# Kernel tuning notes

Hardware: AMD Instinct MI355X
Metric: run time of the kernel (lower is better)

## Reference

```python
import jax, jax.numpy as jnp
import numpy as np

B, L, V, E, H, DOUT = 32, 128, 30000, 300, 512, 5
NUM_STEPS = 5
WINDOW = 1


def setup_inputs() -> dict:
    key = jax.random.key(0)
    ks = jax.random.split(key, 16)
    def p(k, shape, scale=0.02):
        return jax.random.normal(k, shape, jnp.float32) * scale
    tokens = jax.random.randint(ks[0], (B, L), 1, V)
    lengths = jnp.maximum(jax.random.randint(ks[1], (B,), 1, L + 1), 8)
    embed = p(ks[2], (V, E), 0.1).at[0].set(0.0)  # padding_idx=0 row zeroed
    W0 = p(ks[3], (E, H)); b0 = jnp.zeros((H,), jnp.float32)
    Wg = p(ks[4], (3 * H + E + H, 7 * H)); bg = jnp.zeros((7 * H,), jnp.float32)
    Wgf = p(ks[5], (2 * H, H)); bgf = jnp.zeros((H,), jnp.float32)
    Wfi = p(ks[6], (2 * H, H)); bfi = jnp.zeros((H,), jnp.float32)
    Wgo = p(ks[7], (2 * H, H)); bgo = jnp.zeros((H,), jnp.float32)
    W1 = p(ks[8], (H, 2 * H)); b1 = jnp.zeros((2 * H,), jnp.float32)
    W2 = p(ks[9], (2 * H, DOUT)); b2 = jnp.zeros((DOUT,), jnp.float32)
    return dict(tokens=tokens, lengths=lengths, embed=embed, W0=W0, b0=b0,
                Wg=Wg, bg=bg, Wgf=Wgf, bgf=bgf, Wfi=Wfi, bfi=bfi,
                Wgo=Wgo, bgo=bgo, W1=W1, b1=b1, W2=W2, b2=b2)


def _shift_r(a, k):  # h_{i-k}
    return jnp.pad(a, ((0, 0), (k, 0), (0, 0)))[:, :L]


def _shift_l(a, k):  # h_{i+k}
    return jnp.pad(a, ((0, 0), (0, k), (0, 0)))[:, k:]


def reference(tokens, lengths, embed, W0, b0, Wg, bg, Wgf, bgf, Wfi, bfi,
              Wgo, bgo, W1, b1, W2, b2):
    x = embed[tokens]                                   # [B,L,E]
    mask = (jnp.arange(L)[None, :] < lengths[:, None]).astype(x.dtype)[:, :, None]
    lens = jnp.maximum(lengths.astype(x.dtype), 1.0)[:, None]  # [B,1]
    h = jnp.tanh(x @ W0 + b0) * mask                    # word node init [B,L,H]
    c = jnp.zeros_like(h)
    g = jnp.sum(h, axis=1) / lens                       # global node [B,H]
    cg = jnp.zeros_like(g)

    def step(carry, _):
        h, c, g, cg = carry
        hl = sum(_shift_r(h, k) for k in range(1, WINDOW + 1))
        hr = sum(_shift_l(h, k) for k in range(1, WINDOW + 1))
        gb = jnp.broadcast_to(g[:, None, :], h.shape)
        ctx = jnp.concatenate([hl, h, hr, x, gb], axis=-1)  # [B,L,3H+E+H]
        gates = ctx @ Wg + bg                               # [B,L,7H]
        gi, gl, gf, gr, gs, go, gu = jnp.split(gates, 7, axis=-1)
        nrm = jax.nn.softmax(jnp.stack([gi, gl, gf, gr, gs], 0), axis=0)
        i_, l_, f_, r_, s_ = nrm[0], nrm[1], nrm[2], nrm[3], nrm[4]
        o = jax.nn.sigmoid(go)
        u = jnp.tanh(gu)
        c_new = (l_ * _shift_r(c, 1) + f_ * c + r_ * _shift_l(c, 1)
                 + s_ * cg[:, None, :] + i_ * u) * mask
        h_new = o * jnp.tanh(c_new) * mask
        # global (sentence-state) node update
        h_avg = jnp.sum(h_new, axis=1) / lens
        gcat = jnp.concatenate([g, h_avg], axis=-1)         # [B,2H]
        fg = gcat @ Wgf + bgf                               # [B,H]
        og = jax.nn.sigmoid(gcat @ Wgo + bgo)
        fi = jnp.concatenate([jnp.broadcast_to(g[:, None, :], h_new.shape),
                              h_new], axis=-1) @ Wfi + bfi  # [B,L,H]
        slot_logits = jnp.concatenate([fg[:, None, :], fi], axis=1)  # [B,L+1,H]
        slot_mask = jnp.concatenate([jnp.ones((B, 1, 1), x.dtype), mask], axis=1)
        slot_logits = jnp.where(slot_mask > 0, slot_logits, -1e9)
        w = jax.nn.softmax(slot_logits, axis=1)
        cg_new = w[:, 0] * cg + jnp.sum(w[:, 1:] * c_new, axis=1)
        g_new = og * jnp.tanh(cg_new)
        return (h_new, c_new, g_new, cg_new), None

    (h, c, g, cg), _ = jax.lax.scan(step, (h, c, g, cg), None, length=NUM_STEPS)
    logits = jnp.tanh(g @ W1 + b1) @ W2 + b2            # [B,DOUT]
    return jax.nn.log_softmax(logits, axis=-1)
```

## Files before the change

### kernel.cpp

```cpp
#include <hip/hip_runtime.h>
#include <hip/hip_bf16.h>
#include <math.h>

#define B_ 32
#define L_ 128
#define LP 130
#define E_ 300
#define EP 320
#define H_ 512
#define DOUT_ 5
#define NSTEP 5
#define G7 3584
#define KGATES 1856
#define KFI 512

typedef __hip_bfloat16 bf16;
using bf16x8 = __attribute__((ext_vector_type(8))) __bf16;
using f32x4 = __attribute__((ext_vector_type(4))) float;

__device__ __forceinline__ void gload16(const void* g, void* l) {
  __builtin_amdgcn_global_load_lds(
      (const __attribute__((address_space(1))) void*)g,
      (__attribute__((address_space(3))) void*)l, 16, 0, 0);
}

__global__ void fill_zero(float* __restrict__ p, int n) {
  int i = blockIdx.x * blockDim.x + threadIdx.x;
  if (i < n) p[i] = 0.f;
}

__global__ void mask_lens_kernel(const int* __restrict__ lengths,
                                 float* __restrict__ maskf,
                                 float* __restrict__ invlens) {
  int i = blockIdx.x * blockDim.x + threadIdx.x;
  if (i < B_ * L_) {
    int b = i >> 7, l = i & 127;
    maskf[i] = (l < lengths[b]) ? 1.f : 0.f;
    if (l == 0) invlens[b] = 1.f / fmaxf((float)lengths[b], 1.f);
  }
}

__global__ void embed_bf16_kernel(const int* __restrict__ tokens,
                                  const float* __restrict__ embed,
                                  bf16* __restrict__ xb) {
  int i = blockIdx.x * blockDim.x + threadIdx.x;
  if (i >= B_ * L_ * EP) return;
  int e = i % EP, bl = i / EP;
  float v = (e < E_) ? embed[(size_t)tokens[bl] * E_ + e] : 0.f;
  xb[i] = __float2bfloat16(v);
}

__global__ void fill_pad(bf16* __restrict__ hpad) {
  int i = blockIdx.x * blockDim.x + threadIdx.x;
  if (i >= B_ * 2 * H_) return;
  int hh = i & (H_ - 1);
  int r = (i >> 9) & 1, b = i >> 10;
  hpad[((size_t)(b * LP + r * (LP - 1))) * H_ + hh] = __float2bfloat16(0.f);
}

__global__ __launch_bounds__(256) void transpose_to_bf16(
    const float* __restrict__ W, bf16* __restrict__ Wt, int Kreal, int Ncols,
    int dstStride) {
  __shared__ float tile[64][65];
  const int k0 = blockIdx.x * 64, n0 = blockIdx.y * 64;
  const int t = threadIdx.x;
  const int nn = t & 63, kk0 = t >> 6;
#pragma unroll
  for (int p = 0; p < 16; ++p) {
    int kk = kk0 + p * 4;
    int gk = k0 + kk;
    tile[kk][nn] = (gk < Kreal) ? W[(size_t)gk * Ncols + n0 + nn] : 0.f;
  }
  __syncthreads();
#pragma unroll
  for (int p = 0; p < 2; ++p) {
    int r = (t >> 3) + p * 32;
    int kb = (t & 7) * 8;
    union { ushort h[8]; uint4 v; } u;
#pragma unroll
    for (int e = 0; e < 8; ++e) {
      bf16 b = __float2bfloat16(tile[kb + e][r]);
      u.h[e] = *(ushort*)&b;
    }
    *(uint4*)&Wt[(size_t)(n0 + r) * dstStride + k0 + kb] = u.v;
  }
}

__global__ __launch_bounds__(256) void gemm_mfma_init(
    const bf16* __restrict__ A, const bf16* __restrict__ Bt,
    const float* __restrict__ bias, const float* __restrict__ rowscale,
    bf16* __restrict__ Cout, int N, int KP) {
  __shared__ ushort As[128 * 64];
  __shared__ ushort Bs[128 * 64];
  const int tid = threadIdx.x;
  const int lane = tid & 63;
  const int w = tid >> 6;
  const int wr = w >> 1, wc = w & 1;
  const int nbx = gridDim.x;
  const int nwg = nbx * gridDim.y;
  int id = blockIdx.y * nbx + blockIdx.x;
  if ((nwg & 7) == 0) { int q = nwg >> 3; id = (id & 7) * q + (id >> 3); }
  const int bxi = id % nbx, byi = id / nbx;
  const int rowBase = byi * 128, colBase = bxi * 128;
  const int l15 = lane & 15, l4 = lane >> 4;
  f32x4 acc[4][4] = {};

  const bf16* bP[4];
  const bf16* aP[4];
#pragma unroll
  for (int i = 0; i < 4; ++i) {
    int c = tid + 256 * i;
    int r = c >> 3;
    int ql = (c & 7) ^ (r & 7);
    bP[i] = Bt + (size_t)(colBase + r) * KP + ql * 8;
    aP[i] = A + (size_t)(rowBase + r) * KP + ql * 8;
  }

  const int nIter = KP >> 6;
  for (int t = 0; t < nIter; ++t) {
    int k0 = t * 64;
#pragma unroll
    for (int i = 0; i < 4; ++i) {
      gload16(aP[i] + k0, &As[(tid + 256 * i) * 8]);
      gload16(bP[i] + k0, &Bs[(tid + 256 * i) * 8]);
    }
    __syncthreads();
#pragma unroll
    for (int kh = 0; kh < 2; ++kh) {
      bf16x8 aF[4], bF[4];
#pragma unroll
      for (int m = 0; m < 4; ++m) {
        int row = wr * 64 + m * 16 + l15;
        aF[m] = *(const bf16x8*)&As[row * 64 +
                                    (((kh << 2) + l4) ^ (l15 & 7)) * 8];
      }
#pragma unroll
      for (int n = 0; n < 4; ++n) {
        int row = wc * 64 + n * 16 + l15;
        bF[n] = *(const bf16x8*)&Bs[row * 64 +
                                    (((kh << 2) + l4) ^ (l15 & 7)) * 8];
      }
#pragma unroll
      for (int m = 0; m < 4; ++m)
#pragma unroll
        for (int n = 0; n < 4; ++n)
          acc[m][n] = __builtin_amdgcn_mfma_f32_16x16x32_bf16(
              aF[m], bF[n], acc[m][n], 0, 0, 0);
    }
    __syncthreads();
  }

#pragma unroll
  for (int m = 0; m < 4; ++m) {
#pragma unroll
    for (int n = 0; n < 4; ++n) {
      int col = colBase + wc * 64 + n * 16 + l15;
      float bv = bias[col];
#pragma unroll
      for (int j = 0; j < 4; ++j) {
        int row = rowBase + wr * 64 + m * 16 + l4 * 4 + j;
        float v = tanhf(acc[m][n][j] + bv) * rowscale[row];
        size_t oi = ((size_t)((row >> 7) * LP + (row & 127) + 1)) * H_ + col;
        Cout[oi] = __float2bfloat16(v);
      }
    }
  }
}

__global__ __launch_bounds__(256) void gates_gemm(
    const bf16* __restrict__ hpad, const bf16* __restrict__ xb,
    const bf16* __restrict__ Wgt, const float* __restrict__ bias,
    const float* __restrict__ gg, const int* __restrict__ lengths,
    bf16* __restrict__ gatesb) {
  __shared__ ushort As[64 * 64];
  __shared__ ushort Bs[128 * 64];
  const int tid = threadIdx.x;
  const int lane = tid & 63;
  const int w = tid >> 6;
  int id = blockIdx.y * 28 + blockIdx.x;
  id = (id & 7) * 224 + (id >> 3);
  const int bxi = id % 28, byi = id / 28;
  const int b = byi >> 1, lhalf = byi & 1;
  if (lhalf && lengths[b] <= 64) return;
  const int rowBase = byi * 64;
  const int colBase = bxi * 128;
  const int l15 = lane & 15, l4 = lane >> 4;
  f32x4 acc[4][2] = {};

  const int hRowBase = b * LP + lhalf * 64;
  const int blBase = b * L_ + lhalf * 64;
  const bf16* aP[2];
  const bf16* xP[2];
  const bf16* bP[4];
#pragma unroll
  for (int i = 0; i < 2; ++i) {
    int c = tid + 256 * i;
    int r = c >> 3;
    int ql = (c & 7) ^ (r & 7);
    aP[i] = hpad + (size_t)(hRowBase + r) * H_ + ql * 8;
    xP[i] = xb + (size_t)(blBase + r) * EP + ql * 8;
  }
#pragma unroll
  for (int i = 0; i < 4; ++i) {
    int c = tid + 256 * i;
    int r = c >> 3;
    int ql = (c & 7) ^ (r & 7);
    bP[i] = Wgt + (size_t)(colBase + r) * KGATES + ql * 8;
  }

  auto step_ = [&](const bf16* const* ap, int ko, int kb) {
#pragma unroll
    for (int i = 0; i < 2; ++i)
      gload16(ap[i] + ko, &As[(tid + 256 * i) * 8]);
#pragma unroll
    for (int i = 0; i < 4; ++i)
      gload16(bP[i] + kb, &Bs[(tid + 256 * i) * 8]);
    __syncthreads();
#pragma unroll
    for (int kh = 0; kh < 2; ++kh) {
      bf16x8 aF[4], bF[2];
#pragma unroll
      for (int m = 0; m < 4; ++m) {
        int row = m * 16 + l15;
        aF[m] = *(const bf16x8*)&As[row * 64 +
                                    (((kh << 2) + l4) ^ (l15 & 7)) * 8];
      }
#pragma unroll
      for (int n = 0; n < 2; ++n) {
        int row = w * 32 + n * 16 + l15;
        bF[n] = *(const bf16x8*)&Bs[row * 64 +
                                    (((kh << 2) + l4) ^ (l15 & 7)) * 8];
      }
#pragma unroll
      for (int m = 0; m < 4; ++m)
#pragma unroll
        for (int n = 0; n < 2; ++n)
          acc[m][n] = __builtin_amdgcn_mfma_f32_16x16x32_bf16(
              aF[m], bF[n], acc[m][n], 0, 0, 0);
    }
    __syncthreads();
  };

  for (int t = 0; t < 24; ++t) step_(aP, t * 64, t * 64);
  for (int t = 24; t < 29; ++t) step_(xP, (t - 24) * 64, t * 64);

#pragma unroll
  for (int m = 0; m < 4; ++m) {
#pragma unroll
    for (int n = 0; n < 2; ++n) {
      int col = colBase + w * 32 + n * 16 + l15;
      float bv = bias[col] + gg[(size_t)b * G7 + col];
      bf16 tmp[4];
#pragma unroll
      for (int j = 0; j < 4; ++j)
        tmp[j] = __float2bfloat16(acc[m][n][j] + bv);
      int row0 = rowBase + m * 16 + l4 * 4;
      *(uint2*)&gatesb[((size_t)(row0 >> 2) * G7 + col) * 4] = *(uint2*)tmp;
    }
  }
}

__global__ __launch_bounds__(256) void gvec_gemm(
    const float* __restrict__ g, const float* __restrict__ Wgg,
    const float* __restrict__ Wfi, float* __restrict__ gg,
    float* __restrict__ gfi) {
  __shared__ float vin[H_];
  __shared__ float red[4][64];
  const int b = blockIdx.y;
  for (int i = threadIdx.x; i < H_; i += 256) vin[i] = g[(size_t)b * H_ + i];
  __syncthreads();
  const int o = threadIdx.x & 63, kp = threadIdx.x >> 6;
  const bool isg = blockIdx.x < 56;
  const int n0 = isg ? blockIdx.x * 64 : (blockIdx.x - 56) * 64;
  const float* W = isg ? Wgg : Wfi;
  const int ldw = isg ? G7 : H_;
  float acc = 0.f;
#pragma unroll 4
  for (int k = kp * 128; k < kp * 128 + 128; ++k)
    acc = fmaf(vin[k], W[(size_t)k * ldw + n0 + o], acc);
  red[kp][o] = acc;
  __syncthreads();
  if (threadIdx.x < 64) {
    int t = threadIdx.x;
    float v = red[0][t] + red[1][t] + red[2][t] + red[3][t];
    if (isg) gg[(size_t)b * G7 + n0 + t] = v;
    else gfi[(size_t)b * H_ + n0 + t] = v;
  }
}

__global__ __launch_bounds__(256) void fi_slot_kernel(
    const bf16* __restrict__ hpad, const bf16* __restrict__ Wfit,
    const float* __restrict__ bfi, const float* __restrict__ gfi,
    const float* __restrict__ fg, const float* __restrict__ og,
    const bf16* __restrict__ c_new, const float* __restrict__ cg_old,
    const float* __restrict__ maskf, float* __restrict__ cg_new,
    float* __restrict__ g_new) {
  __shared__ __align__(16) char smem[64 * 129 * 4 + 3072];
  ushort* As = (ushort*)smem;
  ushort* Bs = As + 128 * 64;
  float* sfi = (float*)smem;
  float* part = sfi + 64 * 129;

  const int tid = threadIdx.x;
  const int lane = tid & 63;
  const int w = tid >> 6;
  const int b = blockIdx.y;
  const int colBase = blockIdx.x * 64;
  const int l15 = lane & 15, l4 = lane >> 4;
  f32x4 acc[2][4] = {};

  const bf16* aP[4];
  const bf16* bP[2];
#pragma unroll
  for (int i = 0; i < 4; ++i) {
    int c = tid + 256 * i;
    int r = c >> 3;
    int ql = (c & 7) ^ (r & 7);
    aP[i] = hpad + ((size_t)(b * LP + r + 1)) * H_ + ql * 8;
  }
#pragma unroll
  for (int i = 0; i < 2; ++i) {
    int c = tid + 256 * i;
    int r = c >> 3;
    int ql = (c & 7) ^ (r & 7);
    bP[i] = Wfit + (size_t)(colBase + r) * KFI + ql * 8;
  }

  for (int t = 0; t < 8; ++t) {
    int k0 = t * 64;
#pragma unroll
    for (int i = 0; i < 4; ++i)
      gload16(aP[i] + k0, &As[(tid + 256 * i) * 8]);
#pragma unroll
    for (int i = 0; i < 2; ++i)
      gload16(bP[i] + k0, &Bs[(tid + 256 * i) * 8]);
    __syncthreads();
#pragma unroll
    for (int kh = 0; kh < 2; ++kh) {
      bf16x8 aF[2], bF[4];
#pragma unroll
      for (int m = 0; m < 2; ++m) {
        int row = w * 32 + m * 16 + l15;
        aF[m] = *(const bf16x8*)&As[row * 64 +
                                    (((kh << 2) + l4) ^ (l15 & 7)) * 8];
      }
#pragma unroll
      for (int n = 0; n < 4; ++n) {
        int row = n * 16 + l15;
        bF[n] = *(const bf16x8*)&Bs[row * 64 +
                                    (((kh << 2) + l4) ^ (l15 & 7)) * 8];
      }
#pragma unroll
      for (int m = 0; m < 2; ++m)
#pragma unroll
        for (int n = 0; n < 4; ++n)
          acc[m][n] = __builtin_amdgcn_mfma_f32_16x16x32_bf16(
              aF[m], bF[n], acc[m][n], 0, 0, 0);
    }
    __syncthreads();
  }

#pragma unroll
  for (int m = 0; m < 2; ++m) {
#pragma unroll
    for (int n = 0; n < 4; ++n) {
      int hl_ = n * 16 + l15;
      float bv = bfi[colBase + hl_] + gfi[(size_t)b * H_ + colBase + hl_];
#pragma unroll
      for (int j = 0; j < 4; ++j) {
        int l = w * 32 + m * 16 + l4 * 4 + j;
        sfi[hl_ * 129 + l] = acc[m][n][j] + bv;
      }
    }
  }
  __syncthreads();

  {
    int h = tid & 63, q = tid >> 6;
    int hcol = colBase + h;
    const float* mp = maskf + b * L_;
    float m = -3.0e38f, s = 0.f, tv = 0.f;
    for (int l = q * 32; l < q * 32 + 32; ++l) {
      if (mp[l] > 0.f) {
        float xv = sfi[h * 129 + l];
        float vv = __bfloat162float(c_new[((size_t)(b * L_ + l)) * H_ + hcol]);
        float m2 = fmaxf(m, xv);
        float sc = expf(m - m2);
        float e = expf(xv - m2);
        s = s * sc + e;
        tv = tv * sc + e * vv;
        m = m2;
      }
    }
    part[q * 192 + h] = m;
    part[q * 192 + 64 + h] = s;
    part[q * 192 + 128 + h] = tv;
  }
  __syncthreads();
  if (tid < 64) {
    int hcol = colBase + tid;
    int i0 = b * H_ + hcol;
    float mm = part[tid], s0 = part[64 + tid], t0 = part[128 + tid];
#pragma unroll
    for (int k = 1; k < 4; ++k) {
      float mk = part[k * 192 + tid];
      float m2 = fmaxf(mm, mk);
      float e1 = expf(mm - m2), e2 = expf(mk - m2);
      s0 = s0 * e1 + part[k * 192 + 64 + tid] * e2;
      t0 = t0 * e1 + part[k * 192 + 128 + tid] * e2;
      mm = m2;
    }
    float f = fg[i0];
    float m2 = fmaxf(mm, f);
    float ea = expf(mm - m2), eb = expf(f - m2);
    s0 = s0 * ea + eb;
    t0 = t0 * ea + cg_old[i0] * eb;
    float cgn = t0 / s0;
    float gn = og[i0] * tanhf(cgn);
    cg_new[i0] = cgn;
    g_new[i0] = gn;
  }
}

__global__ __launch_bounds__(512) void cell_mean_kernel(
    const bf16* __restrict__ gates, const bf16* __restrict__ c_old,
    const float* __restrict__ cg_old, const float* __restrict__ maskf,
    const float* __restrict__ invlens, bf16* __restrict__ hpad,
    bf16* __restrict__ c_new, float* __restrict__ havg) {
  __shared__ float part[8][64];
  const int b = blockIdx.y;
  const int h0 = blockIdx.x * 64;
  const int hh = threadIdx.x & 63;
  const int lq = threadIdx.x >> 6;
  const int hcol = h0 + hh;
  const float cgv = cg_old[b * H_ + hcol];
  float s = 0.f;
  for (int it = 0; it < 4; ++it) {
    const int gi = it * 8 + lq;
    const int l0 = gi * 4;
    const size_t gbase = ((size_t)(b * 32 + gi) * G7 + hcol) * 4;
    uint2 gv[7];
#pragma unroll
    for (int gt = 0; gt < 7; ++gt)
      gv[gt] = *(const uint2*)&gates[gbase + (size_t)gt * H_ * 4];
    float crow[6];
#pragma unroll
    for (int jj = 0; jj < 6; ++jj) {
      int l = l0 + jj - 1;
      crow[jj] = (l >= 0 && l < L_)
                     ? __bfloat162float(c_old[((size_t)(b * L_ + l)) * H_ + hcol])
                     : 0.f;
    }
#pragma unroll
    for (int j = 0; j < 4; ++j) {
      int l = l0 + j;
      int bl = b * L_ + l;
      float gl_[7];
#pragma unroll
      for (int gt = 0; gt < 7; ++gt) {
        ushort us = ((const ushort*)&gv[gt])[j];
        bf16 hb;
        *(ushort*)&hb = us;
        gl_[gt] = __bfloat162float(hb);
      }
      float m = fmaxf(fmaxf(fmaxf(gl_[0], gl_[1]), fmaxf(gl_[2], gl_[3])),
                      gl_[4]);
      float ei = expf(gl_[0] - m), el = expf(gl_[1] - m),
            ef = expf(gl_[2] - m), er = expf(gl_[3] - m),
            es = expf(gl_[4] - m);
      float inv = 1.f / (ei + el + ef + er + es);
      float o = 1.f / (1.f + expf(-gl_[5]));
      float u = tanhf(gl_[6]);
      float mk = maskf[bl];
      float cn = (el * crow[j] + ef * crow[j + 1] + er * crow[j + 2] +
                  es * cgv + ei * u) * inv * mk;
      float hn = o * tanhf(cn) * mk;
      c_new[(size_t)bl * H_ + hcol] = __float2bfloat16(cn);
      hpad[((size_t)(b * LP + l + 1)) * H_ + hcol] = __float2bfloat16(hn);
      s += hn;
    }
  }
  part[lq][hh] = s;
  __syncthreads();
  if (threadIdx.x < 64) {
    int t = threadIdx.x;
    float v = 0.f;
#pragma unroll
    for (int k = 0; k < 8; ++k) v += part[k][t];
    havg[b * H_ + h0 + t] = v * invlens[b];
  }
}

__global__ __launch_bounds__(256) void reduce_mean_v2(
    const bf16* __restrict__ hpad, const float* __restrict__ invlens,
    float* __restrict__ outf) {
  __shared__ float sm[4][64];
  int b = blockIdx.y, h0 = blockIdx.x * 64;
  int lg = threadIdx.x >> 6, hh = threadIdx.x & 63;
  float s = 0.f;
  for (int l = lg * 32; l < lg * 32 + 32; ++l)
    s += __bfloat162float(hpad[((size_t)(b * LP + l + 1)) * H_ + h0 + hh]);
  sm[lg][hh] = s;
  __syncthreads();
  if (threadIdx.x < 64) {
    int t = threadIdx.x;
    outf[b * H_ + h0 + t] =
        (sm[0][t] + sm[1][t] + sm[2][t] + sm[3][t]) * invlens[b];
  }
}

__global__ __launch_bounds__(256) void batch_vec_gemm(
    const float* __restrict__ in1, int K1, const float* __restrict__ in2,
    int K2, const float* __restrict__ Wa, const float* __restrict__ ba,
    float* __restrict__ outa, int acta, const float* __restrict__ Wb,
    const float* __restrict__ bb, float* __restrict__ outb, int actb, int N) {
  const float* W = (blockIdx.z == 0) ? Wa : Wb;
  const float* bias = (blockIdx.z == 0) ? ba : bb;
  float* op = (blockIdx.z == 0) ? outa : outb;
  int act = (blockIdx.z == 0) ? acta : actb;
  __shared__ float vin[1024];
  __shared__ float red[4][64];
  const int K = K1 + K2;
  const int n0 = blockIdx.x * 64, b = blockIdx.y;
  for (int i = threadIdx.x; i < K; i += 256)
    vin[i] = (i < K1) ? in1[(size_t)b * K1 + i]
                      : in2[(size_t)b * K2 + (i - K1)];
  __syncthreads();
  const int o = threadIdx.x & 63, kp = threadIdx.x >> 6;
  float acc = 0.f;
  const int kc = K >> 2;
#pragma unroll 4
  for (int k = kp * kc; k < kp * kc + kc; ++k)
    acc = fmaf(vin[k], W[(size_t)k * N + n0 + o], acc);
  red[kp][o] = acc;
  __syncthreads();
  if (threadIdx.x < 64) {
    int t = threadIdx.x;
    float v = red[0][t] + red[1][t] + red[2][t] + red[3][t] + bias[n0 + t];
    if (act == 1) v = 1.f / (1.f + expf(-v));
    else if (act == 2) v = tanhf(v);
    op[(size_t)b * N + n0 + t] = v;
  }
}

__global__ __launch_bounds__(256) void final_head_kernel(
    const float* __restrict__ g, const float* __restrict__ W1,
    const float* __restrict__ b1, const float* __restrict__ W2,
    const float* __restrict__ b2, float* __restrict__ out) {
  __shared__ float gv[H_];
  __shared__ float t1s[2 * H_];
  __shared__ float red[256][6];
  const int b = blockIdx.x;
  const int tid = threadIdx.x;
  for (int i = tid; i < H_; i += 256) gv[i] = g[b * H_ + i];
  __syncthreads();
  float accp[4];
#pragma unroll
  for (int p = 0; p < 4; ++p) accp[p] = b1[tid + p * 256];
  for (int k = 0; k < H_; ++k) {
    float gk = gv[k];
#pragma unroll
    for (int p = 0; p < 4; ++p)
      accp[p] = fmaf(gk, W1[(size_t)k * (2 * H_) + tid + p * 256], accp[p]);
  }
#pragma unroll
  for (int p = 0; p < 4; ++p) t1s[tid + p * 256] = tanhf(accp[p]);
  __syncthreads();
  float pd[DOUT_] = {0.f, 0.f, 0.f, 0.f, 0.f};
#pragma unroll
  for (int p = 0; p < 4; ++p) {
    int j = tid + p * 256;
    float tv = t1s[j];
#pragma unroll
    for (int d = 0; d < DOUT_; ++d)
      pd[d] = fmaf(tv, W2[(size_t)j * DOUT_ + d], pd[d]);
  }
#pragma unroll
  for (int d = 0; d < DOUT_; ++d) red[tid][d] = pd[d];
  __syncthreads();
  for (int stride = 128; stride >= 1; stride >>= 1) {
    if (tid < stride) {
#pragma unroll
      for (int d = 0; d < DOUT_; ++d) red[tid][d] += red[tid + stride][d];
    }
    __syncthreads();
  }
  if (tid == 0) {
    float lg[DOUT_];
#pragma unroll
    for (int d = 0; d < DOUT_; ++d) lg[d] = red[0][d] + b2[d];
    float m = lg[0];
#pragma unroll
    for (int d = 1; d < DOUT_; ++d) m = fmaxf(m, lg[d]);
    float s = 0.f;
#pragma unroll
    for (int d = 0; d < DOUT_; ++d) s += expf(lg[d] - m);
    float ls = logf(s);
#pragma unroll
    for (int d = 0; d < DOUT_; ++d) out[b * DOUT_ + d] = lg[d] - m - ls;
  }
}

extern "C" void kernel_launch(void* const* d_in, const int* in_sizes, int n_in,
                              void* d_out, int out_size, void* d_ws,
                              size_t ws_size, hipStream_t stream) {
  (void)in_sizes; (void)n_in; (void)out_size; (void)ws_size;
  const int* tokens = (const int*)d_in[0];
  const int* lengths = (const int*)d_in[1];
  const float* embed = (const float*)d_in[2];
  const float* W0 = (const float*)d_in[3];
  const float* b0 = (const float*)d_in[4];
  const float* Wg = (const float*)d_in[5];
  const float* bg = (const float*)d_in[6];
  const float* Wgf = (const float*)d_in[7];
  const float* bgf = (const float*)d_in[8];
  const float* Wfi = (const float*)d_in[9];
  const float* bfi = (const float*)d_in[10];
  const float* Wgo = (const float*)d_in[11];
  const float* bgo = (const float*)d_in[12];
  const float* W1 = (const float*)d_in[13];
  const float* b1 = (const float*)d_in[14];
  const float* W2 = (const float*)d_in[15];
  const float* b2 = (const float*)d_in[16];
  float* out = (float*)d_out;

  float* ws = (float*)d_ws;
  size_t off = 0;
  auto alloc = [&](size_t nf) {
    float* p = ws + off;
    off += (nf + 7) & ~(size_t)7;
    return p;
  };
  bf16* xb = (bf16*)alloc((size_t)B_ * L_ * EP / 2);
  float* maskf = alloc(B_ * L_);
  float* invlens = alloc(B_);
  bf16* hpad = (bf16*)alloc((size_t)B_ * LP * H_ / 2);
  bf16* cb0 = (bf16*)alloc((size_t)B_ * L_ * H_ / 2);
  bf16* cb1 = (bf16*)alloc((size_t)B_ * L_ * H_ / 2);
  float* g = alloc(B_ * H_);
  float* cgb0 = alloc(B_ * H_);
  float* cgb1 = alloc(B_ * H_);
  float* havg = alloc(B_ * H_);
  float* fg = alloc(B_ * H_);
  float* og = alloc(B_ * H_);
  float* gg = alloc((size_t)B_ * G7);
  float* gfi = alloc(B_ * H_);
  bf16* gatesb = (bf16*)alloc((size_t)B_ * L_ * G7 / 2);
  bf16* Wgt = (bf16*)alloc((size_t)G7 * KGATES / 2);
  bf16* W0t = (bf16*)alloc((size_t)H_ * EP / 2);
  bf16* Wfit = (bf16*)alloc((size_t)H_ * KFI / 2);

  mask_lens_kernel<<<(B_ * L_ + 255) / 256, 256, 0, stream>>>(lengths, maskf,
                                                              invlens);
  embed_bf16_kernel<<<(B_ * L_ * EP + 255) / 256, 256, 0, stream>>>(tokens,
                                                                    embed, xb);
  transpose_to_bf16<<<dim3(24, G7 / 64), 256, 0, stream>>>(Wg, Wgt, 1536, G7,
                                                           KGATES);
  transpose_to_bf16<<<dim3(5, G7 / 64), 256, 0, stream>>>(
      Wg + (size_t)1536 * G7, Wgt + 1536, 300, G7, KGATES);
  transpose_to_bf16<<<dim3(5, H_ / 64), 256, 0, stream>>>(W0, W0t, 300, H_, EP);
  transpose_to_bf16<<<dim3(8, H_ / 64), 256, 0, stream>>>(
      Wfi + (size_t)H_ * H_, Wfit, H_, H_, KFI);
  fill_pad<<<(B_ * 2 * H_ + 255) / 256, 256, 0, stream>>>(hpad);
  gemm_mfma_init<<<dim3(H_ / 128, (B_ * L_) / 128), 256, 0, stream>>>(
      xb, W0t, b0, maskf, hpad, H_, EP);
  reduce_mean_v2<<<dim3(8, B_), 256, 0, stream>>>(hpad, invlens, g);
  fill_zero<<<(B_ * L_ * H_ / 2 + 255) / 256, 256, 0, stream>>>(
      (float*)cb0, B_ * L_ * H_ / 2);
  fill_zero<<<(B_ * H_ + 255) / 256, 256, 0, stream>>>(cgb0, B_ * H_);

  bf16* cb[2] = {cb0, cb1};
  float* cgb[2] = {cgb0, cgb1};
  int cur = 0;
  for (int step = 0; step < NSTEP; ++step) {
    int nxt = cur ^ 1;
    gvec_gemm<<<dim3(64, B_), 256, 0, stream>>>(g, Wg + (size_t)1836 * G7,
                                                Wfi, gg, gfi);
    gates_gemm<<<dim3(28, 64), 256, 0, stream>>>(hpad, xb, Wgt, bg, gg,
                                                 lengths, gatesb);
    cell_mean_kernel<<<dim3(H_ / 64, B_), 512, 0, stream>>>(
        gatesb, cb[cur], cgb[cur], maskf, invlens, hpad, cb[nxt], havg);
    batch_vec_gemm<<<dim3(8, B_, 2), 256, 0, stream>>>(
        g, H_, havg, H_, Wgf, bgf, fg, 0, Wgo, bgo, og, 1, H_);
    fi_slot_kernel<<<dim3(H_ / 64, B_), 256, 0, stream>>>(
        hpad, Wfit, bfi, gfi, fg, og, cb[nxt], cgb[cur], maskf, cgb[nxt], g);
    cur = nxt;
  }
  final_head_kernel<<<B_, 256, 0, stream>>>(g, W1, b1, W2, b2, out);
}
```

Measured before the change: 765.5 us.

## Fuse gates GEMM with cell update via gate-interleaved weight columns

The gates GEMM now reorders weight rows so each block computes all seven gates for 16 hidden units, then applies the LSTM-style cell update and partial sentence-average directly in the epilogue. This removes the bf16 gates intermediate buffer and the separate cell kernel's round trip through memory. It double-buffers hpad to avoid read/write hazards, and skips padded-length work in fi_slot_kernel. The new tile shape (64x112) uses fewer MFMA per A fragment, which may lower GEMM efficiency.

```diff
diff --git a/kernel.cpp b/kernel.cpp
--- a/kernel.cpp
+++ b/kernel.cpp
@@ -50,12 +50,14 @@
   xb[i] = __float2bfloat16(v);
 }
 
-__global__ void fill_pad(bf16* __restrict__ hpad) {
+__global__ void fill_pad2(bf16* __restrict__ hpad0, bf16* __restrict__ hpad1) {
   int i = blockIdx.x * blockDim.x + threadIdx.x;
   if (i >= B_ * 2 * H_) return;
   int hh = i & (H_ - 1);
   int r = (i >> 9) & 1, b = i >> 10;
-  hpad[((size_t)(b * LP + r * (LP - 1))) * H_ + hh] = __float2bfloat16(0.f);
+  size_t oi = ((size_t)(b * LP + r * (LP - 1))) * H_ + hh;
+  hpad0[oi] = __float2bfloat16(0.f);
+  hpad1[oi] = __float2bfloat16(0.f);
 }
 
 __global__ __launch_bounds__(256) void transpose_to_bf16(
@@ -167,25 +169,31 @@
   }
 }
 
-__global__ __launch_bounds__(256) void gates_gemm(
-    const bf16* __restrict__ hpad, const bf16* __restrict__ xb,
-    const bf16* __restrict__ Wgt, const float* __restrict__ bias,
+__global__ __launch_bounds__(256) void gates_cell_kernel(
+    const bf16* __restrict__ hpad_old, const bf16* __restrict__ xb,
+    const bf16* __restrict__ Wgt, const float* __restrict__ bg,
     const float* __restrict__ gg, const int* __restrict__ lengths,
-    bf16* __restrict__ gatesb) {
-  __shared__ ushort As[64 * 64];
-  __shared__ ushort Bs[128 * 64];
+    const bf16* __restrict__ c_old, const float* __restrict__ cg_old,
+    bf16* __restrict__ c_new, bf16* __restrict__ hpad_new,
+    float* __restrict__ havg_part) {
+  __shared__ __align__(16) char smem[64 * 113 * 4 + 16 * 16 * 4];
+  ushort* As = (ushort*)smem;
+  ushort* Bs = As + 64 * 64;
+  float* sfi = (float*)smem;
+  float* red = sfi + 64 * 113;
+
   const int tid = threadIdx.x;
   const int lane = tid & 63;
   const int w = tid >> 6;
-  int id = blockIdx.y * 28 + blockIdx.x;
-  id = (id & 7) * 224 + (id >> 3);
-  const int bxi = id % 28, byi = id / 28;
+  int worig = blockIdx.y * 32 + blockIdx.x;
+  int id = (worig & 7) * 256 + (worig >> 3);
+  const int bxi = id >> 6;
+  const int byi = id & 63;
   const int b = byi >> 1, lhalf = byi & 1;
-  if (lhalf && lengths[b] <= 64) return;
-  const int rowBase = byi * 64;
-  const int colBase = bxi * 128;
+  const int len = lengths[b];
+  if (lhalf && len <= 64) return;
   const int l15 = lane & 15, l4 = lane >> 4;
-  f32x4 acc[4][2] = {};
+  f32x4 acc[7] = {};
 
   const int hRowBase = b * LP + lhalf * 64;
   const int blBase = b * L_ + lhalf * 64;
@@ -197,15 +205,17 @@
     int c = tid + 256 * i;
     int r = c >> 3;
     int ql = (c & 7) ^ (r & 7);
-    aP[i] = hpad + (size_t)(hRowBase + r) * H_ + ql * 8;
+    aP[i] = hpad_old + (size_t)(hRowBase + r) * H_ + ql * 8;
     xP[i] = xb + (size_t)(blBase + r) * EP + ql * 8;
   }
 #pragma unroll
   for (int i = 0; i < 4; ++i) {
     int c = tid + 256 * i;
-    int r = c >> 3;
+    int r = (c < 896) ? (c >> 3) : 0;
     int ql = (c & 7) ^ (r & 7);
-    bP[i] = Wgt + (size_t)(colBase + r) * KGATES + ql * 8;
+    int j = bxi * 112 + r;
+    int src = (j % 7) * 512 + (j / 7);
+    bP[i] = Wgt + (size_t)src * KGATES + ql * 8;
   }
 
   auto step_ = [&](const bf16* const* ap, int ko, int kb) {
@@ -213,30 +223,26 @@
     for (int i = 0; i < 2; ++i)
       gload16(ap[i] + ko, &As[(tid + 256 * i) * 8]);
 #pragma unroll
-    for (int i = 0; i < 4; ++i)
+    for (int i = 0; i < 3; ++i)
       gload16(bP[i] + kb, &Bs[(tid + 256 * i) * 8]);
+    if (tid < 128) gload16(bP[3] + kb, &Bs[(tid + 768) * 8]);
     __syncthreads();
 #pragma unroll
     for (int kh = 0; kh < 2; ++kh) {
-      bf16x8 aF[4], bF[2];
-#pragma unroll
-      for (int m = 0; m < 4; ++m) {
-        int row = m * 16 + l15;
-        aF[m] = *(const bf16x8*)&As[row * 64 +
+      int arow = w * 16 + l15;
+      bf16x8 aF = *(const bf16x8*)&As[arow * 64 +
+                                      (((kh << 2) + l4) ^ (l15 & 7)) * 8];
+      bf16x8 bF[7];
+#pragma unroll
+      for (int n = 0; n < 7; ++n) {
+        int brow = n * 16 + l15;
+        bF[n] = *(const bf16x8*)&Bs[brow * 64 +
                                     (((kh << 2) + l4) ^ (l15 & 7)) * 8];
       }
 #pragma unroll
-      for (int n = 0; n < 2; ++n) {
-        int row = w * 32 + n * 16 + l15;
-        bF[n] = *(const bf16x8*)&Bs[row * 64 +
-                                    (((kh << 2) + l4) ^ (l15 & 7)) * 8];
-      }
-#pragma unroll
-      for (int m = 0; m < 4; ++m)
-#pragma unroll
-        for (int n = 0; n < 2; ++n)
-          acc[m][n] = __builtin_amdgcn_mfma_f32_16x16x32_bf16(
-              aF[m], bF[n], acc[m][n], 0, 0, 0);
+      for (int n = 0; n < 7; ++n)
+        acc[n] = __builtin_amdgcn_mfma_f32_16x16x32_bf16(aF, bF[n], acc[n],
+                                                         0, 0, 0);
     }
     __syncthreads();
   };
@@ -245,18 +251,61 @@
   for (int t = 24; t < 29; ++t) step_(xP, (t - 24) * 64, t * 64);
 
 #pragma unroll
-  for (int m = 0; m < 4; ++m) {
-#pragma unroll
-    for (int n = 0; n < 2; ++n) {
-      int col = colBase + w * 32 + n * 16 + l15;
-      float bv = bias[col] + gg[(size_t)b * G7 + col];
-      bf16 tmp[4];
-#pragma unroll
-      for (int j = 0; j < 4; ++j)
-        tmp[j] = __float2bfloat16(acc[m][n][j] + bv);
-      int row0 = rowBase + m * 16 + l4 * 4;
-      *(uint2*)&gatesb[((size_t)(row0 >> 2) * G7 + col) * 4] = *(uint2*)tmp;
-    }
+  for (int n = 0; n < 7; ++n)
+#pragma unroll
+    for (int j = 0; j < 4; ++j)
+      sfi[(w * 16 + l4 * 4 + j) * 113 + n * 16 + l15] = acc[n][j];
+  __syncthreads();
+
+  const int hloc = tid & 15;
+  const int lgrp = tid >> 4;
+  const int hglob = bxi * 16 + hloc;
+  float bv[7];
+#pragma unroll
+  for (int g = 0; g < 7; ++g)
+    bv[g] = bg[g * 512 + hglob] + gg[(size_t)b * G7 + g * 512 + hglob];
+  const float cgv = cg_old[b * H_ + hglob];
+  float s = 0.f;
+#pragma unroll
+  for (int it = 0; it < 4; ++it) {
+    int loc = lgrp + it * 16;
+    int lglob = lhalf * 64 + loc;
+    int bl = b * L_ + lglob;
+    size_t coi = (size_t)bl * H_ + hglob;
+    size_t hoi = ((size_t)(b * LP + lglob + 1)) * H_ + hglob;
+    if (lglob >= len) {
+      c_new[coi] = __float2bfloat16(0.f);
+      hpad_new[hoi] = __float2bfloat16(0.f);
+      continue;
+    }
+    float gl_[7];
+#pragma unroll
+    for (int g = 0; g < 7; ++g) gl_[g] = sfi[loc * 113 + hloc * 7 + g] + bv[g];
+    float m = fmaxf(fmaxf(fmaxf(gl_[0], gl_[1]), fmaxf(gl_[2], gl_[3])),
+                    gl_[4]);
+    float ei = expf(gl_[0] - m), el = expf(gl_[1] - m), ef = expf(gl_[2] - m),
+          er = expf(gl_[3] - m), es = expf(gl_[4] - m);
+    float inv = 1.f / (ei + el + ef + er + es);
+    float o = 1.f / (1.f + expf(-gl_[5]));
+    float u = tanhf(gl_[6]);
+    float cprev = (lglob >= 1)
+                      ? __bfloat162float(c_old[coi - H_]) : 0.f;
+    float ccur = __bfloat162float(c_old[coi]);
+    float cnext = (lglob < L_ - 1)
+                      ? __bfloat162float(c_old[coi + H_]) : 0.f;
+    float cn = (el * cprev + ef * ccur + er * cnext + es * cgv + ei * u) * inv;
+    float hn = o * tanhf(cn);
+    c_new[coi] = __float2bfloat16(cn);
+    hpad_new[hoi] = __float2bfloat16(hn);
+    s += hn;
+  }
+  red[hloc * 16 + lgrp] = s;
+  __syncthreads();
+  if (tid < 16) {
+    float v = 0.f;
+#pragma unroll
+    for (int k = 0; k < 16; ++k) v += red[tid * 16 + k];
+    havg_part[(size_t)lhalf * B_ * H_ + (size_t)b * H_ + bxi * 16 + tid] = v;
   }
 }
 
@@ -288,13 +337,47 @@
   }
 }
 
+__global__ __launch_bounds__(256) void gnode_vec(
+    const float* __restrict__ g, const float* __restrict__ havg_part,
+    const float* __restrict__ invlens, const float* __restrict__ Wgf,
+    const float* __restrict__ bgf, float* __restrict__ fg,
+    const float* __restrict__ Wgo, const float* __restrict__ bgo,
+    float* __restrict__ og) {
+  const int z = blockIdx.z;
+  const float* W = z ? Wgo : Wgf;
+  const float* bias = z ? bgo : bgf;
+  float* op = z ? og : fg;
+  __shared__ float vin[1024];
+  __shared__ float red[4][64];
+  const int n0 = blockIdx.x * 64, b = blockIdx.y;
+  const float il = invlens[b];
+  for (int i = threadIdx.x; i < 1024; i += 256)
+    vin[i] = (i < 512) ? g[(size_t)b * H_ + i]
+                       : (havg_part[(size_t)b * H_ + (i - 512)] +
+                          havg_part[(size_t)(B_ + b) * H_ + (i - 512)]) * il;
+  __syncthreads();
+  const int o = threadIdx.x & 63, kp = threadIdx.x >> 6;
+  float acc = 0.f;
+#pragma unroll 4
+  for (int k = kp * 256; k < kp * 256 + 256; ++k)
+    acc = fmaf(vin[k], W[(size_t)k * H_ + n0 + o], acc);
+  red[kp][o] = acc;
+  __syncthreads();
+  if (threadIdx.x < 64) {
+    int t = threadIdx.x;
+    float v = red[0][t] + red[1][t] + red[2][t] + red[3][t] + bias[n0 + t];
+    if (z) v = 1.f / (1.f + expf(-v));
+    op[(size_t)b * H_ + n0 + t] = v;
+  }
+}
+
 __global__ __launch_bounds__(256) void fi_slot_kernel(
     const bf16* __restrict__ hpad, const bf16* __restrict__ Wfit,
     const float* __restrict__ bfi, const float* __restrict__ gfi,
     const float* __restrict__ fg, const float* __restrict__ og,
     const bf16* __restrict__ c_new, const float* __restrict__ cg_old,
-    const float* __restrict__ maskf, float* __restrict__ cg_new,
-    float* __restrict__ g_new) {
+    const float* __restrict__ maskf, const int* __restrict__ lengths,
+    float* __restrict__ cg_new, float* __restrict__ g_new) {
   __shared__ __align__(16) char smem[64 * 129 * 4 + 3072];
   ushort* As = (ushort*)smem;
   ushort* Bs = As + 128 * 64;
@@ -305,6 +388,8 @@
   const int lane = tid & 63;
   const int w = tid >> 6;
   const int b = blockIdx.y;
+  const int len = lengths[b];
+  const bool wactive = len > w * 32;
   const int colBase = blockIdx.x * 64;
   const int l15 = lane & 15, l4 = lane >> 4;
   f32x4 acc[2][4] = {};
@@ -335,41 +420,45 @@
     for (int i = 0; i < 2; ++i)
       gload16(bP[i] + k0, &Bs[(tid + 256 * i) * 8]);
     __syncthreads();
-#pragma unroll
-    for (int kh = 0; kh < 2; ++kh) {
-      bf16x8 aF[2], bF[4];
-#pragma unroll
-      for (int m = 0; m < 2; ++m) {
-        int row = w * 32 + m * 16 + l15;
-        aF[m] = *(const bf16x8*)&As[row * 64 +
-                                    (((kh << 2) + l4) ^ (l15 & 7)) * 8];
+    if (wactive) {
+#pragma unroll
+      for (int kh = 0; kh < 2; ++kh) {
+        bf16x8 aF[2], bF[4];
+#pragma unroll
+        for (int m = 0; m < 2; ++m) {
+          int row = w * 32 + m * 16 + l15;
+          aF[m] = *(const bf16x8*)&As[row * 64 +
+                                      (((kh << 2) + l4) ^ (l15 & 7)) * 8];
+        }
+#pragma unroll
+        for (int n = 0; n < 4; ++n) {
+          int row = n * 16 + l15;
+          bF[n] = *(const bf16x8*)&Bs[row * 64 +
+                                      (((kh << 2) + l4) ^ (l15 & 7)) * 8];
+        }
+#pragma unroll
+        for (int m = 0; m < 2; ++m)
+#pragma unroll
+          for (int n = 0; n < 4; ++n)
+            acc[m][n] = __builtin_amdgcn_mfma_f32_16x16x32_bf16(
+                aF[m], bF[n], acc[m][n], 0, 0, 0);
       }
+    }
+    __syncthreads();
+  }
+
+  if (wactive) {
+#pragma unroll
+    for (int m = 0; m < 2; ++m) {
 #pragma unroll
       for (int n = 0; n < 4; ++n) {
-        int row = n * 16 + l15;
-        bF[n] = *(const bf16x8*)&Bs[row * 64 +
-                                    (((kh << 2) + l4) ^ (l15 & 7)) * 8];
-      }
-#pragma unroll
-      for (int m = 0; m < 2; ++m)
-#pragma unroll
-        for (int n = 0; n < 4; ++n)
-          acc[m][n] = __builtin_amdgcn_mfma_f32_16x16x32_bf16(
-              aF[m], bF[n], acc[m][n], 0, 0, 0);
-    }
-    __syncthreads();
-  }
-
-#pragma unroll
-  for (int m = 0; m < 2; ++m) {
-#pragma unroll
-    for (int n = 0; n < 4; ++n) {
-      int hl_ = n * 16 + l15;
-      float bv = bfi[colBase + hl_] + gfi[(size_t)b * H_ + colBase + hl_];
-#pragma unroll
-      for (int j = 0; j < 4; ++j) {
-        int l = w * 32 + m * 16 + l4 * 4 + j;
-        sfi[hl_ * 129 + l] = acc[m][n][j] + bv;
+        int hl_ = n * 16 + l15;
+        float bv = bfi[colBase + hl_] + gfi[(size_t)b * H_ + colBase + hl_];
+#pragma unroll
+        for (int j = 0; j < 4; ++j) {
+          int l = w * 32 + m * 16 + l4 * 4 + j;
+          sfi[hl_ * 129 + l] = acc[m][n][j] + bv;
+        }
       }
     }
   }
@@ -380,16 +469,19 @@
     int hcol = colBase + h;
     const float* mp = maskf + b * L_;
     float m = -3.0e38f, s = 0.f, tv = 0.f;
-    for (int l = q * 32; l < q * 32 + 32; ++l) {
-      if (mp[l] > 0.f) {
-        float xv = sfi[h * 129 + l];
-        float vv = __bfloat162float(c_new[((size_t)(b * L_ + l)) * H_ + hcol]);
-        float m2 = fmaxf(m, xv);
-        float sc = expf(m - m2);
-        float e = expf(xv - m2);
-        s = s * sc + e;
-        tv = tv * sc + e * vv;
-        m = m2;
+    if (len > q * 32) {
+      for (int l = q * 32; l < q * 32 + 32; ++l) {
+        if (mp[l] > 0.f) {
+          float xv = sfi[h * 129 + l];
+          float vv =
+              __bfloat162float(c_new[((size_t)(b * L_ + l)) * H_ + hcol]);
+          float m2 = fmaxf(m, xv);
+          float sc = expf(m - m2);
+          float e = expf(xv - m2);
+          s = s * sc + e;
+          tv = tv * sc + e * vv;
+          m = m2;
+        }
       }
     }
     part[q * 192 + h] = m;
@@ -419,75 +511,6 @@
     float gn = og[i0] * tanhf(cgn);
     cg_new[i0] = cgn;
     g_new[i0] = gn;
-  }
-}
-
-__global__ __launch_bounds__(512) void cell_mean_kernel(
-    const bf16* __restrict__ gates, const bf16* __restrict__ c_old,
-    const float* __restrict__ cg_old, const float* __restrict__ maskf,
-    const float* __restrict__ invlens, bf16* __restrict__ hpad,
-    bf16* __restrict__ c_new, float* __restrict__ havg) {
-  __shared__ float part[8][64];
-  const int b = blockIdx.y;
-  const int h0 = blockIdx.x * 64;
-  const int hh = threadIdx.x & 63;
-  const int lq = threadIdx.x >> 6;
-  const int hcol = h0 + hh;
-  const float cgv = cg_old[b * H_ + hcol];
-  float s = 0.f;
-  for (int it = 0; it < 4; ++it) {
-    const int gi = it * 8 + lq;
-    const int l0 = gi * 4;
-    const size_t gbase = ((size_t)(b * 32 + gi) * G7 + hcol) * 4;
-    uint2 gv[7];
-#pragma unroll
-    for (int gt = 0; gt < 7; ++gt)
-      gv[gt] = *(const uint2*)&gates[gbase + (size_t)gt * H_ * 4];
-    float crow[6];
-#pragma unroll
-    for (int jj = 0; jj < 6; ++jj) {
-      int l = l0 + jj - 1;
-      crow[jj] = (l >= 0 && l < L_)
-                     ? __bfloat162float(c_old[((size_t)(b * L_ + l)) * H_ + hcol])
-                     : 0.f;
-    }
-#pragma unroll
-    for (int j = 0; j < 4; ++j) {
-      int l = l0 + j;
-      int bl = b * L_ + l;
-      float gl_[7];
-#pragma unroll
-      for (int gt = 0; gt < 7; ++gt) {
-        ushort us = ((const ushort*)&gv[gt])[j];
-        bf16 hb;
-        *(ushort*)&hb = us;
-        gl_[gt] = __bfloat162float(hb);
-      }
-      float m = fmaxf(fmaxf(fmaxf(gl_[0], gl_[1]), fmaxf(gl_[2], gl_[3])),
-                      gl_[4]);
-      float ei = expf(gl_[0] - m), el = expf(gl_[1] - m),
-            ef = expf(gl_[2] - m), er = expf(gl_[3] - m),
-            es = expf(gl_[4] - m);
-      float inv = 1.f / (ei + el + ef + er + es);
-      float o = 1.f / (1.f + expf(-gl_[5]));
-      float u = tanhf(gl_[6]);
-      float mk = maskf[bl];
-      float cn = (el * crow[j] + ef * crow[j + 1] + er * crow[j + 2] +
-                  es * cgv + ei * u) * inv * mk;
-      float hn = o * tanhf(cn) * mk;
-      c_new[(size_t)bl * H_ + hcol] = __float2bfloat16(cn);
-      hpad[((size_t)(b * LP + l + 1)) * H_ + hcol] = __float2bfloat16(hn);
-      s += hn;
-    }
-  }
-  part[lq][hh] = s;
-  __syncthreads();
-  if (threadIdx.x < 64) {
-    int t = threadIdx.x;
-    float v = 0.f;
-#pragma unroll
-    for (int k = 0; k < 8; ++k) v += part[k][t];
-    havg[b * H_ + h0 + t] = v * invlens[b];
   }
 }
 
@@ -506,40 +529,6 @@
     int t = threadIdx.x;
     outf[b * H_ + h0 + t] =
         (sm[0][t] + sm[1][t] + sm[2][t] + sm[3][t]) * invlens[b];
-  }
-}
-
-__global__ __launch_bounds__(256) void batch_vec_gemm(
-    const float* __restrict__ in1, int K1, const float* __restrict__ in2,
-    int K2, const float* __restrict__ Wa, const float* __restrict__ ba,
-    float* __restrict__ outa, int acta, const float* __restrict__ Wb,
-    const float* __restrict__ bb, float* __restrict__ outb, int actb, int N) {
-  const float* W = (blockIdx.z == 0) ? Wa : Wb;
-  const float* bias = (blockIdx.z == 0) ? ba : bb;
-  float* op = (blockIdx.z == 0) ? outa : outb;
-  int act = (blockIdx.z == 0) ? acta : actb;
-  __shared__ float vin[1024];
-  __shared__ float red[4][64];
-  const int K = K1 + K2;
-  const int n0 = blockIdx.x * 64, b = blockIdx.y;
-  for (int i = threadIdx.x; i < K; i += 256)
-    vin[i] = (i < K1) ? in1[(size_t)b * K1 + i]
-                      : in2[(size_t)b * K2 + (i - K1)];
-  __syncthreads();
-  const int o = threadIdx.x & 63, kp = threadIdx.x >> 6;
-  float acc = 0.f;
-  const int kc = K >> 2;
-#pragma unroll 4
-  for (int k = kp * kc; k < kp * kc + kc; ++k)
-    acc = fmaf(vin[k], W[(size_t)k * N + n0 + o], acc);
-  red[kp][o] = acc;
-  __syncthreads();
-  if (threadIdx.x < 64) {
-    int t = threadIdx.x;
-    float v = red[0][t] + red[1][t] + red[2][t] + red[3][t] + bias[n0 + t];
-    if (act == 1) v = 1.f / (1.f + expf(-v));
-    else if (act == 2) v = tanhf(v);
-    op[(size_t)b * N + n0 + t] = v;
   }
 }
 
@@ -634,18 +623,18 @@
   bf16* xb = (bf16*)alloc((size_t)B_ * L_ * EP / 2);
   float* maskf = alloc(B_ * L_);
   float* invlens = alloc(B_);
-  bf16* hpad = (bf16*)alloc((size_t)B_ * LP * H_ / 2);
+  bf16* hpad0 = (bf16*)alloc((size_t)B_ * LP * H_ / 2);
+  bf16* hpad1 = (bf16*)alloc((size_t)B_ * LP * H_ / 2);
   bf16* cb0 = (bf16*)alloc((size_t)B_ * L_ * H_ / 2);
   bf16* cb1 = (bf16*)alloc((size_t)B_ * L_ * H_ / 2);
   float* g = alloc(B_ * H_);
   float* cgb0 = alloc(B_ * H_);
   float* cgb1 = alloc(B_ * H_);
-  float* havg = alloc(B_ * H_);
+  float* havg_part = alloc((size_t)2 * B_ * H_);
   float* fg = alloc(B_ * H_);
   float* og = alloc(B_ * H_);
   float* gg = alloc((size_t)B_ * G7);
   float* gfi = alloc(B_ * H_);
-  bf16* gatesb = (bf16*)alloc((size_t)B_ * L_ * G7 / 2);
   bf16* Wgt = (bf16*)alloc((size_t)G7 * KGATES / 2);
   bf16* W0t = (bf16*)alloc((size_t)H_ * EP / 2);
   bf16* Wfit = (bf16*)alloc((size_t)H_ * KFI / 2);
@@ -661,29 +650,32 @@
   transpose_to_bf16<<<dim3(5, H_ / 64), 256, 0, stream>>>(W0, W0t, 300, H_, EP);
   transpose_to_bf16<<<dim3(8, H_ / 64), 256, 0, stream>>>(
       Wfi + (size_t)H_ * H_, Wfit, H_, H_, KFI);
-  fill_pad<<<(B_ * 2 * H_ + 255) / 256, 256, 0, stream>>>(hpad);
+  fill_pad2<<<(B_ * 2 * H_ + 255) / 256, 256, 0, stream>>>(hpad0, hpad1);
   gemm_mfma_init<<<dim3(H_ / 128, (B_ * L_) / 128), 256, 0, stream>>>(
-      xb, W0t, b0, maskf, hpad, H_, EP);
-  reduce_mean_v2<<<dim3(8, B_), 256, 0, stream>>>(hpad, invlens, g);
+      xb, W0t, b0, maskf, hpad0, H_, EP);
+  reduce_mean_v2<<<dim3(8, B_), 256, 0, stream>>>(hpad0, invlens, g);
   fill_zero<<<(B_ * L_ * H_ / 2 + 255) / 256, 256, 0, stream>>>(
       (float*)cb0, B_ * L_ * H_ / 2);
   fill_zero<<<(B_ * H_ + 255) / 256, 256, 0, stream>>>(cgb0, B_ * H_);
+  fill_zero<<<(B_ * H_ + 255) / 256, 256, 0, stream>>>(havg_part + B_ * H_,
+                                                       B_ * H_);
 
   bf16* cb[2] = {cb0, cb1};
+  bf16* hp[2] = {hpad0, hpad1};
   float* cgb[2] = {cgb0, cgb1};
   int cur = 0;
   for (int step = 0; step < NSTEP; ++step) {
     int nxt = cur ^ 1;
     gvec_gemm<<<dim3(64, B_), 256, 0, stream>>>(g, Wg + (size_t)1836 * G7,
                                                 Wfi, gg, gfi);
-    gates_gemm<<<dim3(28, 64), 256, 0, stream>>>(hpad, xb, Wgt, bg, gg,
-                                                 lengths, gatesb);
-    cell_mean_kernel<<<dim3(H_ / 64, B_), 512, 0, stream>>>(
-        gatesb, cb[cur], cgb[cur], maskf, invlens, hpad, cb[nxt], havg);
-    batch_vec_gemm<<<dim3(8, B_, 2), 256, 0, stream>>>(
-        g, H_, havg, H_, Wgf, bgf, fg, 0, Wgo, bgo, og, 1, H_);
-    fi_slot_kernel<<<dim3(H_ / 64, B_), 256, 0, stream>>>(
-        hpad, Wfit, bfi, gfi, fg, og, cb[nxt], cgb[cur], maskf, cgb[nxt], g);
+    gates_cell_kernel<<<dim3(32, 64), 256, 0, stream>>>(
+        hp[cur], xb, Wgt, bg, gg, lengths, cb[cur], cgb[cur], cb[nxt],
+        hp[nxt], havg_part);
+    gnode_vec<<<dim3(8, B_, 2), 256, 0, stream>>>(
+        g, havg_part, invlens, Wgf, bgf, fg, Wgo, bgo, og);
+    fi_slot_kernel<<<dim3(8, B_), 256, 0, stream>>>(
+        hp[nxt], Wfit, bfi, gfi, fg, og, cb[nxt], cgb[cur], maskf, lengths,
+        cgb[nxt], g);
     cur = nxt;
   }
   final_head_kernel<<<B_, 256, 0, stream>>>(g, W1, b1, W2, b2, out);
```

Result: faster. 708.6 us (-7.4%).
